# Optimization experiments

Hardware: AMD Instinct MI355X
Metric: run time of the kernel (lower is better)

The kernel has to match this reference:

```python
import jax, jax.numpy as jnp
import numpy as np

# Module constants (match init_kwargs)
L = 4096          # input_size / output_length (mod=0)
WIN = 25          # window_size
STRIDE = 1
PAD = (WIN - 1) // 2          # auto padding = 12
PADDED = L + 2 * PAD          # 4120
OUT = L                       # mod=0 -> same length


def _band_mask():
    # mask[i, j] = True for j in [i*stride, i*stride + window)
    starts = jnp.arange(OUT)[:, None] * STRIDE          # [OUT,1]
    cols = jnp.arange(PADDED)[None, :]                   # [1,PADDED]
    return (cols >= starts) & (cols < starts + WIN)      # [OUT,PADDED] bool


def setup_inputs() -> dict:
    key = jax.random.key(0)
    kx, kw, kb = jax.random.split(key, 3)
    x = jax.random.normal(kx, (32, L, 64), dtype=jnp.float32)
    W = jax.random.normal(kw, (OUT, PADDED), dtype=jnp.float32) * 0.02
    b = jax.random.normal(kb, (OUT,), dtype=jnp.float32) * 0.02
    return {"x": x, "W": W, "b": b}


def reference(x, W, b):
    # x: [B, L, C] -> [B, C, L]
    xc = jnp.transpose(x, (0, 2, 1))
    # Replicate-edge style padding: copy first PAD and last PAD steps (not reversed)
    xp = jnp.concatenate([xc[:, :, :PAD], xc, xc[:, :, -PAD:]], axis=-1)  # [B,C,PADDED]
    mask = _band_mask().astype(W.dtype)
    Wm = W * mask                                                          # banded weight
    out = jnp.einsum('bcp,op->bco', xp, Wm) + b                            # [B,C,OUT]
    return jnp.transpose(out, (0, 2, 1))                                   # [B,OUT,C]
```

## Files before the change

### kernel.cpp

```cpp
#include <hip/hip_runtime.h>


typedef __attribute__((ext_vector_type(8))) short short8;
typedef __attribute__((ext_vector_type(4))) float f32x4;

constexpr int Lseq = 4096;
constexpr int C    = 64;
constexpr int WIN  = 25;
constexpr int PAD  = 12;
constexpr int O_B  = 128;
constexpr int PWIN = 176;
constexpr int PLX  = 184;
constexpr int WROW = 28;
constexpr int NB   = 32;

__device__ __forceinline__ ushort f2bf(float f) {
    union { float f; uint u; } v; v.f = f;
    uint r = v.u + 0x7FFFu + ((v.u >> 16) & 1u);
    return (ushort)(r >> 16);
}

__device__ __forceinline__ int tap_to_t(int q) {
    int t = (q < PAD) ? q : ((q < Lseq + PAD) ? q - PAD : q - 2 * PAD);
    return t > Lseq - 1 ? Lseq - 1 : t;
}

__global__ __launch_bounds__(256) void lll_one(const float* __restrict__ x,
                                               const float* __restrict__ W,
                                               const float* __restrict__ bias,
                                               float* __restrict__ out) {
    __shared__ ushort x_lds[C * PLX];
    __shared__ float  w_band[O_B * WROW];

    const int bid   = blockIdx.x;
    const int tile  = bid >> 5;
    const int b     = bid & 31;
    const int blk_o = tile * O_B;

    const int tid  = threadIdx.x;
    const int lane = tid & 63;
    const int w    = tid >> 6;
    const int m    = lane & 15;
    const int quad = lane >> 4;

    {
        const int row = tid >> 1, h = tid & 1;
        const float* wr = W + (size_t)(blk_o + row) * 4121 + h * 12;
        float v[13];
#pragma unroll
        for (int i = 0; i < 13; ++i) v[i] = wr[i];
        float* dst = &w_band[row * WROW + h * 12];
#pragma unroll
        for (int i = 0; i < 13; ++i) dst[i] = v[i];
    }

    const float4* xb = (const float4*)(x + (size_t)b * Lseq * C);
#pragma unroll
    for (int s = 0; s < 2; ++s) {
        const int u = tid + 256 * s;
        if (u < 16 * (PWIN / 8)) {
            const int c4 = u & 15, oct = u >> 4, p0 = oct * 8;
            float4 f[8];
#pragma unroll
            for (int i = 0; i < 8; ++i)
                f[i] = xb[(size_t)tap_to_t(blk_o + p0 + i) * 16 + c4];
#pragma unroll
            for (int ch = 0; ch < 4; ++ch) {
                short8 pk;
#pragma unroll
                for (int i = 0; i < 8; ++i) {
                    const float v = (ch == 0) ? f[i].x : (ch == 1) ? f[i].y
                                  : (ch == 2) ? f[i].z : f[i].w;
                    pk[i] = (short)f2bf(v);
                }
                *(short8*)&x_lds[(c4 * 4 + ch) * PLX + p0] = pk;
            }
        }
    }
    __syncthreads();

    short8 afrag[2][2];
#pragma unroll
    for (int it = 0; it < 2; ++it) {
        const int row = (w * 2 + it) * 16 + m;
#pragma unroll
        for (int cch = 0; cch < 2; ++cch) {
            const int j0 = cch * 32 + quad * 8 - m;
            short8 pk;
#pragma unroll
            for (int e = 0; e < 8; ++e) {
                const int j  = j0 + e;
                const int jc = min(max(j, 0), WIN - 1);
                const float f = w_band[row * WROW + jc];
                pk[e] = (short)f2bf((j == jc) ? f : 0.f);
            }
            afrag[it][cch] = pk;
        }
    }

    float* ob = out + (size_t)b * Lseq * C;
#pragma unroll
    for (int it = 0; it < 2; ++it) {
        const int t16 = w * 2 + it;
        const int o0  = blk_o + t16 * 16;

        f32x4 acc[4];
        {
            const float4 bv = *((const float4*)(bias + o0) + quad);
            const float bb[4] = {bv.x, bv.y, bv.z, bv.w};
#pragma unroll
            for (int r = 0; r < 4; ++r)
#pragma unroll
                for (int g = 0; g < 4; ++g) acc[g][r] = bb[r];
        }

#pragma unroll
        for (int cch = 0; cch < 2; ++cch) {
            const int poff = t16 * 16 + cch * 32 + quad * 8;
#pragma unroll
            for (int g = 0; g < 4; ++g) {
                short8 bf = *(const short8*)&x_lds[(m + 16 * g) * PLX + poff];
                acc[g] = __builtin_amdgcn_mfma_f32_16x16x32_bf16(afrag[it][cch], bf,
                                                                 acc[g], 0, 0, 0);
            }
        }

#pragma unroll
        for (int g = 0; g < 4; ++g)
#pragma unroll
            for (int r = 0; r < 4; ++r)
                ob[(size_t)(o0 + quad * 4 + r) * C + m + 16 * g] = acc[g][r];
    }
}

extern "C" void kernel_launch(void* const* d_in, const int* in_sizes, int n_in,
                              void* d_out, int out_size, void* d_ws, size_t ws_size,
                              hipStream_t stream) {
    const float* x    = (const float*)d_in[0];
    const float* W    = (const float*)d_in[1];
    const float* bias = (const float*)d_in[2];
    float*       out  = (float*)d_out;

    lll_one<<<NB * (Lseq / O_B), 256, 0, stream>>>(x, W, bias, out);
}
```

Baseline: 17.82 us.

## Process two batches per block with double-buffered LDS to amortize weight setup

```diff
diff --git a/kernel.cpp b/kernel.cpp
--- a/kernel.cpp
+++ b/kernel.cpp
@@ -25,16 +25,78 @@
     return t > Lseq - 1 ? Lseq - 1 : t;
 }
 
-__global__ __launch_bounds__(256) void lll_one(const float* __restrict__ x,
-                                               const float* __restrict__ W,
-                                               const float* __restrict__ bias,
-                                               float* __restrict__ out) {
-    __shared__ ushort x_lds[C * PLX];
+__device__ __forceinline__ void pack_write(const float4 f[2][8], bool has2,
+                                           ushort* xl, int tid) {
+#pragma unroll
+    for (int s = 0; s < 2; ++s) {
+        if (s == 1 && !has2) break;
+        const int u = tid + 256 * s;
+        const int c4 = u & 15, oct = u >> 4, p0 = oct * 8;
+#pragma unroll
+        for (int ch = 0; ch < 4; ++ch) {
+            short8 pk;
+#pragma unroll
+            for (int i = 0; i < 8; ++i) {
+                const float v = (ch == 0) ? f[s][i].x : (ch == 1) ? f[s][i].y
+                              : (ch == 2) ? f[s][i].z : f[s][i].w;
+                pk[i] = (short)f2bf(v);
+            }
+            *(short8*)&xl[(c4 * 4 + ch) * PLX + p0] = pk;
+        }
+    }
+}
+
+__device__ __forceinline__ void compute_store(const ushort* __restrict__ xl,
+                                              const short8 af[2][2],
+                                              const float* __restrict__ bias,
+                                              float* __restrict__ ob,
+                                              int blk_o, int w, int m, int quad) {
+#pragma unroll
+    for (int it = 0; it < 2; ++it) {
+        const int t16 = w * 2 + it;
+        const int o0  = blk_o + t16 * 16;
+
+        f32x4 acc[4];
+        {
+            const float4 bv = *((const float4*)(bias + o0) + quad);
+            const float bb[4] = {bv.x, bv.y, bv.z, bv.w};
+#pragma unroll
+            for (int r = 0; r < 4; ++r)
+#pragma unroll
+                for (int g = 0; g < 4; ++g) acc[g][r] = bb[r];
+        }
+
+#pragma unroll
+        for (int cch = 0; cch < 2; ++cch) {
+            const int poff = t16 * 16 + cch * 32 + quad * 8;
+#pragma unroll
+            for (int g = 0; g < 4; ++g) {
+                short8 bf = *(const short8*)&xl[(m + 16 * g) * PLX + poff];
+                acc[g] = __builtin_amdgcn_mfma_f32_16x16x32_bf16(af[it][cch], bf,
+                                                                 acc[g], 0, 0, 0);
+            }
+        }
+
+#pragma unroll
+        for (int g = 0; g < 4; ++g)
+#pragma unroll
+            for (int r = 0; r < 4; ++r)
+                ob[(size_t)(o0 + quad * 4 + r) * C + m + 16 * g] = acc[g][r];
+    }
+}
+
+__global__ __launch_bounds__(256) void lll_db(const float* __restrict__ x,
+                                              const float* __restrict__ W,
+                                              const float* __restrict__ bias,
+                                              float* __restrict__ out) {
+    __shared__ ushort x_lds[2][C * PLX];
     __shared__ float  w_band[O_B * WROW];
 
     const int bid   = blockIdx.x;
-    const int tile  = bid >> 5;
-    const int b     = bid & 31;
+    const int tile  = bid >> 4;
+    const int pr    = bid & 15;
+    const int b0    = pr;
+    const int b1    = pr + 16;
     const int blk_o = tile * O_B;
 
     const int tid  = threadIdx.x;
@@ -54,29 +116,24 @@
         for (int i = 0; i < 13; ++i) dst[i] = v[i];
     }
 
-    const float4* xb = (const float4*)(x + (size_t)b * Lseq * C);
+    const bool has2 = tid < 16 * (PWIN / 8) - 256;
+    const float4* xb0 = (const float4*)(x + (size_t)b0 * Lseq * C);
+    const float4* xb1 = (const float4*)(x + (size_t)b1 * Lseq * C);
+
+    float4 fA[2][8], fB[2][8];
 #pragma unroll
     for (int s = 0; s < 2; ++s) {
+        if (s == 1 && !has2) break;
         const int u = tid + 256 * s;
-        if (u < 16 * (PWIN / 8)) {
-            const int c4 = u & 15, oct = u >> 4, p0 = oct * 8;
-            float4 f[8];
+        const int c4 = u & 15, oct = u >> 4, p0 = oct * 8;
 #pragma unroll
-            for (int i = 0; i < 8; ++i)
-                f[i] = xb[(size_t)tap_to_t(blk_o + p0 + i) * 16 + c4];
-#pragma unroll
-            for (int ch = 0; ch < 4; ++ch) {
-                short8 pk;
-#pragma unroll
-                for (int i = 0; i < 8; ++i) {
-                    const float v = (ch == 0) ? f[i].x : (ch == 1) ? f[i].y
-                                  : (ch == 2) ? f[i].z : f[i].w;
-                    pk[i] = (short)f2bf(v);
-                }
-                *(short8*)&x_lds[(c4 * 4 + ch) * PLX + p0] = pk;
-            }
+        for (int i = 0; i < 8; ++i) {
+            const size_t off = (size_t)tap_to_t(blk_o + p0 + i) * 16 + c4;
+            fA[s][i] = xb0[off];
+            fB[s][i] = xb1[off];
         }
     }
+    pack_write(fA, has2, &x_lds[0][0], tid);
     __syncthreads();
 
     short8 afrag[2][2];
@@ -98,39 +155,13 @@
         }
     }
 
-    float* ob = out + (size_t)b * Lseq * C;
-#pragma unroll
-    for (int it = 0; it < 2; ++it) {
-        const int t16 = w * 2 + it;
-        const int o0  = blk_o + t16 * 16;
+    compute_store(&x_lds[0][0], afrag, bias,
+                  out + (size_t)b0 * Lseq * C, blk_o, w, m, quad);
 
-        f32x4 acc[4];
-        {
-            const float4 bv = *((const float4*)(bias + o0) + quad);
-            const float bb[4] = {bv.x, bv.y, bv.z, bv.w};
-#pragma unroll
-            for (int r = 0; r < 4; ++r)
-#pragma unroll
-                for (int g = 0; g < 4; ++g) acc[g][r] = bb[r];
-        }
-
-#pragma unroll
-        for (int cch = 0; cch < 2; ++cch) {
-            const int poff = t16 * 16 + cch * 32 + quad * 8;
-#pragma unroll
-            for (int g = 0; g < 4; ++g) {
-                short8 bf = *(const short8*)&x_lds[(m + 16 * g) * PLX + poff];
-                acc[g] = __builtin_amdgcn_mfma_f32_16x16x32_bf16(afrag[it][cch], bf,
-                                                                 acc[g], 0, 0, 0);
-            }
-        }
-
-#pragma unroll
-        for (int g = 0; g < 4; ++g)
-#pragma unroll
-            for (int r = 0; r < 4; ++r)
-                ob[(size_t)(o0 + quad * 4 + r) * C + m + 16 * g] = acc[g][r];
-    }
+    pack_write(fB, has2, &x_lds[1][0], tid);
+    __syncthreads();
+    compute_store(&x_lds[1][0], afrag, bias,
+                  out + (size_t)b1 * Lseq * C, blk_o, w, m, quad);
 }
 
 extern "C" void kernel_launch(void* const* d_in, const int* in_sizes, int n_in,
@@ -141,5 +172,5 @@
     const float* bias = (const float*)d_in[2];
     float*       out  = (float*)d_out;
 
-    lll_one<<<NB * (Lseq / O_B), 256, 0, stream>>>(x, W, bias, out);
+    lll_db<<<(Lseq / O_B) * (NB / 2), 256, 0, stream>>>(x, W, bias, out);
 }
```

New measurement: 18.98 us. 6.5% more time.

## Split channels across two blocks and issue x loads before weight staging

Applied to the files above, without the earlier changes.

```diff
diff --git a/kernel.cpp b/kernel.cpp
--- a/kernel.cpp
+++ b/kernel.cpp
@@ -6,6 +6,7 @@
 
 constexpr int Lseq = 4096;
 constexpr int C    = 64;
+constexpr int CH   = 32;
 constexpr int WIN  = 25;
 constexpr int PAD  = 12;
 constexpr int O_B  = 128;
@@ -25,16 +26,18 @@
     return t > Lseq - 1 ? Lseq - 1 : t;
 }
 
-__global__ __launch_bounds__(256) void lll_one(const float* __restrict__ x,
-                                               const float* __restrict__ W,
-                                               const float* __restrict__ bias,
-                                               float* __restrict__ out) {
-    __shared__ ushort x_lds[C * PLX];
+__global__ __launch_bounds__(256) void lll_cs(const float* __restrict__ x,
+                                              const float* __restrict__ W,
+                                              const float* __restrict__ bias,
+                                              float* __restrict__ out) {
+    __shared__ ushort x_lds[CH * PLX];
     __shared__ float  w_band[O_B * WROW];
 
     const int bid   = blockIdx.x;
-    const int tile  = bid >> 5;
-    const int b     = bid & 31;
+    const int tile  = bid >> 6;
+    const int sub   = bid & 63;
+    const int b     = sub >> 1;
+    const int chalf = sub & 1;
     const int blk_o = tile * O_B;
 
     const int tid  = threadIdx.x;
@@ -42,6 +45,16 @@
     const int w    = tid >> 6;
     const int m    = lane & 15;
     const int quad = lane >> 4;
+
+    const bool hasx = tid < 8 * (PWIN / 8);
+    const int c8 = tid & 7, p0 = (tid >> 3) * 8;
+    const float4* xb = (const float4*)(x + (size_t)b * Lseq * C);
+    float4 f[8];
+    if (hasx) {
+#pragma unroll
+        for (int i = 0; i < 8; ++i)
+            f[i] = xb[(size_t)tap_to_t(blk_o + p0 + i) * 16 + chalf * 8 + c8];
+    }
 
     {
         const int row = tid >> 1, h = tid & 1;
@@ -54,27 +67,17 @@
         for (int i = 0; i < 13; ++i) dst[i] = v[i];
     }
 
-    const float4* xb = (const float4*)(x + (size_t)b * Lseq * C);
+    if (hasx) {
 #pragma unroll
-    for (int s = 0; s < 2; ++s) {
-        const int u = tid + 256 * s;
-        if (u < 16 * (PWIN / 8)) {
-            const int c4 = u & 15, oct = u >> 4, p0 = oct * 8;
-            float4 f[8];
+        for (int ch = 0; ch < 4; ++ch) {
+            short8 pk;
 #pragma unroll
-            for (int i = 0; i < 8; ++i)
-                f[i] = xb[(size_t)tap_to_t(blk_o + p0 + i) * 16 + c4];
-#pragma unroll
-            for (int ch = 0; ch < 4; ++ch) {
-                short8 pk;
-#pragma unroll
-                for (int i = 0; i < 8; ++i) {
-                    const float v = (ch == 0) ? f[i].x : (ch == 1) ? f[i].y
-                                  : (ch == 2) ? f[i].z : f[i].w;
-                    pk[i] = (short)f2bf(v);
-                }
-                *(short8*)&x_lds[(c4 * 4 + ch) * PLX + p0] = pk;
+            for (int i = 0; i < 8; ++i) {
+                const float v = (ch == 0) ? f[i].x : (ch == 1) ? f[i].y
+                              : (ch == 2) ? f[i].z : f[i].w;
+                pk[i] = (short)f2bf(v);
             }
+            *(short8*)&x_lds[(c8 * 4 + ch) * PLX + p0] = pk;
         }
     }
     __syncthreads();
@@ -91,8 +94,8 @@
             for (int e = 0; e < 8; ++e) {
                 const int j  = j0 + e;
                 const int jc = min(max(j, 0), WIN - 1);
-                const float f = w_band[row * WROW + jc];
-                pk[e] = (short)f2bf((j == jc) ? f : 0.f);
+                const float g = w_band[row * WROW + jc];
+                pk[e] = (short)f2bf((j == jc) ? g : 0.f);
             }
             afrag[it][cch] = pk;
         }
@@ -104,21 +107,21 @@
         const int t16 = w * 2 + it;
         const int o0  = blk_o + t16 * 16;
 
-        f32x4 acc[4];
+        f32x4 acc[2];
         {
             const float4 bv = *((const float4*)(bias + o0) + quad);
             const float bb[4] = {bv.x, bv.y, bv.z, bv.w};
 #pragma unroll
             for (int r = 0; r < 4; ++r)
 #pragma unroll
-                for (int g = 0; g < 4; ++g) acc[g][r] = bb[r];
+                for (int g = 0; g < 2; ++g) acc[g][r] = bb[r];
         }
 
 #pragma unroll
         for (int cch = 0; cch < 2; ++cch) {
             const int poff = t16 * 16 + cch * 32 + quad * 8;
 #pragma unroll
-            for (int g = 0; g < 4; ++g) {
+            for (int g = 0; g < 2; ++g) {
                 short8 bf = *(const short8*)&x_lds[(m + 16 * g) * PLX + poff];
                 acc[g] = __builtin_amdgcn_mfma_f32_16x16x32_bf16(afrag[it][cch], bf,
                                                                  acc[g], 0, 0, 0);
@@ -126,10 +129,11 @@
         }
 
 #pragma unroll
-        for (int g = 0; g < 4; ++g)
+        for (int g = 0; g < 2; ++g)
 #pragma unroll
             for (int r = 0; r < 4; ++r)
-                ob[(size_t)(o0 + quad * 4 + r) * C + m + 16 * g] = acc[g][r];
+                ob[(size_t)(o0 + quad * 4 + r) * C + chalf * CH + m + 16 * g]
+                    = acc[g][r];
     }
 }
 
@@ -141,5 +145,5 @@
     const float* bias = (const float*)d_in[2];
     float*       out  = (float*)d_out;
 
-    lll_one<<<NB * (Lseq / O_B), 256, 0, stream>>>(x, W, bias, out);
+    lll_cs<<<(Lseq / O_B) * NB * 2, 256, 0, stream>>>(x, W, bias, out);
 }
```

Measured after the change: 18.80 us. 1.05x slower.
